# Kernel tuning notes

Hardware: AMD Instinct MI355X
Metric: run time of the kernel (lower is better)

## Reference

```python
import jax, jax.numpy as jnp
import numpy as np

DIM = 1024
HEADS = 16
B, N = 4, 2048


def setup_inputs() -> dict:
    key = jax.random.key(0)
    ks = jax.random.split(key, 6)
    scale = DIM ** -0.5
    return {
        "x": jax.random.normal(ks[0], (B, N, DIM), dtype=jnp.float32),
        "mask": jax.random.randint(ks[1], (B, N, N), 0, 2) > 0,
        "Wqkv": jax.random.normal(ks[2], (DIM, 3 * DIM), dtype=jnp.float32) * scale,
        "bqkv": jax.random.normal(ks[3], (3 * DIM,), dtype=jnp.float32) * 0.02,
        "Wproj": jax.random.normal(ks[4], (DIM, DIM), dtype=jnp.float32) * scale,
        "bproj": jax.random.normal(ks[5], (DIM,), dtype=jnp.float32) * 0.02,
    }


def reference(x, mask, Wqkv, bqkv, Wproj, bproj):
    Bs, Ns, C = x.shape
    H = HEADS
    D = C // H
    scale = D ** -0.5
    qkv = x @ Wqkv + bqkv                       # [B, N, 3C]
    qkv = qkv.reshape(Bs, Ns, 3, H, D)          # split (three h d)
    q, k, v = jnp.moveaxis(qkv, 2, 0)           # each [B, N, H, D]
    q = q.transpose(0, 2, 1, 3)                 # [B, H, N, D]
    k = k.transpose(0, 2, 1, 3)
    v = v.transpose(0, 2, 1, 3)
    attn = jnp.einsum("bhnd,bhmd->bhnm", q, k) * scale  # [B, H, N, N]
    attn = jnp.where(mask[:, None, :, :], -jnp.inf, attn)
    attn = jax.nn.softmax(attn, axis=-1)
    out = jnp.einsum("bhnm,bhmd->bhnd", attn, v)        # [B, H, N, D]
    out = out.transpose(0, 2, 1, 3).reshape(Bs, Ns, C)  # [B, N, C]
    return out @ Wproj + bproj
```

## Files before the change

### kernel.cpp

```cpp
#include <hip/hip_runtime.h>
#include <cstdint>
#include <cstddef>

constexpr int kC = 1024;
constexpr int kH = 16;
constexpr int kB = 4;
constexpr int kN = 2048;
constexpr int kD = 64;

#define KQ_SCALE 0.18033688011112042f

typedef unsigned short u16;
typedef unsigned int   u32;
typedef unsigned long long u64;
typedef __bf16 v8bf  __attribute__((ext_vector_type(8)));
typedef __bf16 v4bf  __attribute__((ext_vector_type(4)));
typedef float  v4f   __attribute__((ext_vector_type(4)));
typedef u16    u16x8 __attribute__((ext_vector_type(8)));
typedef u16    u16x4 __attribute__((ext_vector_type(4)));
typedef u32    u32x4 __attribute__((ext_vector_type(4)));

__device__ inline u16 f2bf(float f) {
    union { float f; unsigned u; } v; v.f = f;
    unsigned r = v.u + 0x7FFFu + ((v.u >> 16) & 1u);
    return (u16)(r >> 16);
}

__device__ inline float fast_exp2(float x) {
#if __has_builtin(__builtin_amdgcn_exp2f)
    return __builtin_amdgcn_exp2f(x);
#else
    return __expf(x * 0.6931471805599453f);
#endif
}

__device__ inline void gl2lds16(const u16* g, u16* l) {
    __builtin_amdgcn_global_load_lds(
        (const __attribute__((address_space(1))) void*)g,
        (__attribute__((address_space(3))) void*)l, 16, 0, 0);
}

__global__ __launch_bounds__(256) void cast_bf16_kernel(
    const float* __restrict__ in, u16* __restrict__ outp)
{
    const int i = blockIdx.x * 256 + threadIdx.x;
    const float4 f = ((const float4*)in)[i];
    u16x4 o;
    o.x = f2bf(f.x); o.y = f2bf(f.y); o.z = f2bf(f.z); o.w = f2bf(f.w);
    ((u16x4*)outp)[i] = o;
}

__global__ __launch_bounds__(256) void tpose_cast_kernel(
    const float* __restrict__ W, u16* __restrict__ Wt, int R, int Cc)
{
    __shared__ u16 tile[64][65];
    const int c0 = blockIdx.x * 64;
    const int r0 = blockIdx.y * 64;
    const int t  = threadIdx.x;
#pragma unroll
    for (int it = 0; it < 16; ++it) {
        const int r = it * 4 + (t >> 6);
        const int c = t & 63;
        tile[c][r] = f2bf(W[(size_t)(r0 + r) * Cc + c0 + c]);
    }
    __syncthreads();
#pragma unroll
    for (int it = 0; it < 16; ++it) {
        const int rr = it * 4 + (t >> 6);
        const int cc = t & 63;
        Wt[(size_t)(c0 + rr) * R + r0 + cc] = tile[rr][cc];
    }
}

__global__ __launch_bounds__(256) void maskpack_kernel(
    const int* __restrict__ mask, u32* __restrict__ bits)
{
    const int seg  = blockIdx.x * 4 + (threadIdx.x >> 6);
    const int lane = threadIdx.x & 63;
    const size_t row = (size_t)(seg >> 5);
    const int s = seg & 31;
    const int m = mask[row * kN + s * 64 + lane];
    const u64 bal = __ballot(m != 0);
    if (lane == 0) ((u64*)bits)[row * 32 + s] = bal;
}

template <int MODE>
__global__ __launch_bounds__(256) void gemm_mfma_kernel(
    const u16* __restrict__ A, const u16* __restrict__ Bt,
    const float* __restrict__ bias, float* __restrict__ Cout,
    u16* __restrict__ qOut, u16* __restrict__ kOut, u16* __restrict__ vOut,
    int M, int N, int K)
{
    __shared__ u16 As[128 * 32];
    __shared__ u16 Bs[128 * 32];
    const int t    = threadIdx.x;
    const int w    = t >> 6;
    const int lane = t & 63;
    const int quad = lane >> 4;
    const int l16  = lane & 15;
    const int m0   = blockIdx.y * 128;
    const int n0   = blockIdx.x * 128;

    const int sr = lane >> 2;
    const int sk = (lane & 3) * 8;
    const u16* Ag0 = A  + (size_t)(m0 + 32 * w      + sr) * K + sk;
    const u16* Ag1 = A  + (size_t)(m0 + 32 * w + 16 + sr) * K + sk;
    const u16* Bg0 = Bt + (size_t)(n0 + 32 * w      + sr) * K + sk;
    const u16* Bg1 = Bt + (size_t)(n0 + 32 * w + 16 + sr) * K + sk;
    u16* Al0 = &As[(32 * w)      * 32];
    u16* Al1 = &As[(32 * w + 16) * 32];
    u16* Bl0 = &Bs[(32 * w)      * 32];
    u16* Bl1 = &Bs[(32 * w + 16) * 32];

    v4f acc[4][4];
#pragma unroll
    for (int r = 0; r < 4; ++r)
#pragma unroll
        for (int c = 0; c < 4; ++c) acc[r][c] = (v4f){0.f, 0.f, 0.f, 0.f};

    const int mrow = (w >> 1) * 64;
    const int ncol = (w & 1) * 64;

    for (int k0 = 0; k0 < K; k0 += 32) {
        __syncthreads();
        gl2lds16(Ag0 + k0, Al0);
        gl2lds16(Ag1 + k0, Al1);
        gl2lds16(Bg0 + k0, Bl0);
        gl2lds16(Bg1 + k0, Bl1);
        __syncthreads();

        v8bf af[4], bfr[4];
#pragma unroll
        for (int r = 0; r < 4; ++r)
            af[r] = *(const v8bf*)(&As[(mrow + r * 16 + l16) * 32 + quad * 8]);
#pragma unroll
        for (int c = 0; c < 4; ++c)
            bfr[c] = *(const v8bf*)(&Bs[(ncol + c * 16 + l16) * 32 + quad * 8]);
#pragma unroll
        for (int r = 0; r < 4; ++r)
#pragma unroll
            for (int c = 0; c < 4; ++c)
                acc[r][c] = __builtin_amdgcn_mfma_f32_16x16x32_bf16(
                    af[r], bfr[c], acc[r][c], 0, 0, 0);
    }

#pragma unroll
    for (int r = 0; r < 4; ++r) {
#pragma unroll
        for (int c = 0; c < 4; ++c) {
            const int col = n0 + ncol + c * 16 + l16;
            const float bv = bias[col];
#pragma unroll
            for (int reg = 0; reg < 4; ++reg) {
                const int row = m0 + mrow + r * 16 + quad * 4 + reg;
                float val = acc[r][c][reg] + bv;
                if (MODE == 0) {
                    Cout[(size_t)row * N + col] = val;
                } else {
                    const int which = col >> 10;
                    const int rem   = col & 1023;
                    const int h     = rem >> 6;
                    const int d     = rem & 63;
                    const int b     = row >> 11;
                    const int n     = row & 2047;
                    if (which == 0) val *= KQ_SCALE;
                    u16* dst = (which == 0) ? qOut : (which == 1) ? kOut : vOut;
                    dst[(((size_t)(b * kH + h)) * kN + n) * kD + d] = f2bf(val);
                }
            }
        }
    }
}

__global__ __launch_bounds__(256, 2) void attn_mfma_kernel(
    const u16* __restrict__ q, const u16* __restrict__ k,
    const u16* __restrict__ v, const u32* __restrict__ mbits,
    u16* __restrict__ out)
{
    __shared__ u16 Ks[128 * 64];
    __shared__ u16 Vt[64 * 128];

    const int t    = threadIdx.x;
    const int w    = t >> 6;
    const int lane = t & 63;
    const int quad = lane >> 4;
    const int l16  = lane & 15;

    const int bh    = blockIdx.x >> 4;
    const int tile0 = (blockIdx.x & 15) * 128;
    const int b     = bh >> 4;
    const int h     = bh & 15;

    const u16* qb = q + (size_t)bh * kN * kD;
    const u16* kb = k + (size_t)bh * kN * kD;
    const u16* vb = v + (size_t)bh * kN * kD;

    const int qrow0 = tile0 + w * 32 + l16;
    const int qrow1 = qrow0 + 16;
    v8bf qf[2][2];
    qf[0][0] = *(const v8bf*)(qb + (size_t)qrow0 * kD + quad * 8);
    qf[0][1] = *(const v8bf*)(qb + (size_t)qrow0 * kD + 32 + quad * 8);
    qf[1][0] = *(const v8bf*)(qb + (size_t)qrow1 * kD + quad * 8);
    qf[1][1] = *(const v8bf*)(qb + (size_t)qrow1 * kD + 32 + quad * 8);

    const int skr  = t >> 1;
    const int skh  = t & 1;
    const int vg   = t >> 4;
    const int vdq  = t & 15;
    const int vrow0 = (vg >> 2) * 32 + (vg & 3) * 4;

    const u16* kp = kb + (size_t)skr * kD + skh * 32;
    const u16* vp = vb + (size_t)vrow0 * kD + vdq * 4;
    const uint4* mp0 = (const uint4*)(mbits + ((size_t)b * kN + qrow0) * 64);
    const uint4* mp1 = (const uint4*)(mbits + ((size_t)b * kN + qrow1) * 64);

    u16x8 kpre[4];
    u16x4 vpre[8];
    uint4 mpre0, mpre1;
    auto issue_prefetch = [&]() {
#pragma unroll
        for (int i = 0; i < 4; ++i)
            kpre[i] = *(const u16x8*)(kp + i * 8);
#pragma unroll
        for (int i = 0; i < 8; ++i)
            vpre[i] = *(const u16x4*)(vp + (i < 4 ? i * 64 : 1024 + (i - 4) * 64));
        mpre0 = *mp0; mpre1 = *mp1;
        kp += 128 * kD; vp += 128 * kD; ++mp0; ++mp1;
    };

    v8bf onesf;
#pragma unroll
    for (int j = 0; j < 8; ++j) onesf[j] = (__bf16)1.0f;

    v4f oacc[2][4];
    v4f rsacc[2];
#pragma unroll
    for (int qs = 0; qs < 2; ++qs) {
        rsacc[qs] = (v4f){0.f, 0.f, 0.f, 0.f};
#pragma unroll
        for (int i = 0; i < 4; ++i) oacc[qs][i] = (v4f){0.f, 0.f, 0.f, 0.f};
    }

    issue_prefetch();

    for (int kt = 0; kt < kN / 128; ++kt) {
        __syncthreads();

        {
            const int cb = skh * 4;
            u16* drow = &Ks[skr * 64];
#pragma unroll
            for (int i = 0; i < 4; ++i)
                *(u16x8*)(&drow[((cb + i) ^ (skr & 7)) * 8]) = kpre[i];
        }
        {
#pragma unroll
            for (int dd = 0; dd < 4; ++dd) {
                const int d = vdq * 4 + dd;
                u16x8 col;
#pragma unroll
                for (int j = 0; j < 8; ++j) col[j] = vpre[j][dd];
                *(u16x8*)(&Vt[d * 128 + ((vg ^ (d & 15)) * 8)]) = col;
            }
        }
        const uint4 mc0 = mpre0, mc1 = mpre1;
        if (kt + 1 < kN / 128) issue_prefetch();
        __syncthreads();

        const u32 mwa[2][4] = {{mc0.x, mc0.y, mc0.z, mc0.w},
                               {mc1.x, mc1.y, mc1.z, mc1.w}};
        u32 pf[2][4][4];

#pragma unroll
        for (int nb = 0; nb < 8; ++nb) {
            const int krow = nb * 16 + l16;
            const v8bf kf0 = *(const v8bf*)(&Ks[krow * 64 + ((quad       ^ (krow & 7)) * 8)]);
            const v8bf kf1 = *(const v8bf*)(&Ks[krow * 64 + (((quad + 4) ^ (krow & 7)) * 8)]);
#pragma unroll
            for (int qs = 0; qs < 2; ++qs) {
                v4f s = (v4f){0.f, 0.f, 0.f, 0.f};
                s = __builtin_amdgcn_mfma_f32_16x16x32_bf16(kf0, qf[qs][0], s, 0, 0, 0);
                s = __builtin_amdgcn_mfma_f32_16x16x32_bf16(kf1, qf[qs][1], s, 0, 0, 0);

                const u32 m4 = (mwa[qs][nb >> 1] >> ((nb & 1) * 16 + quad * 4)) & 0xFu;
                float e0 = fast_exp2(s[0]);
                float e1 = fast_exp2(s[1]);
                float e2 = fast_exp2(s[2]);
                float e3 = fast_exp2(s[3]);
                e0 = (m4 & 1u) ? 0.f : e0;
                e1 = (m4 & 2u) ? 0.f : e1;
                e2 = (m4 & 4u) ? 0.f : e2;
                e3 = (m4 & 8u) ? 0.f : e3;

                union { v4bf v; u32 u[2]; } bu;
                bu.v = (v4bf){(__bf16)e0, (__bf16)e1, (__bf16)e2, (__bf16)e3};
                pf[qs][nb >> 1][(nb & 1) * 2 + 0] = bu.u[0];
                pf[qs][nb >> 1][(nb & 1) * 2 + 1] = bu.u[1];
            }
        }

        v8bf pa[2][4];
#pragma unroll
        for (int qs = 0; qs < 2; ++qs)
#pragma unroll
            for (int ks = 0; ks < 4; ++ks) {
                u32x4 t4 = {pf[qs][ks][0], pf[qs][ks][1], pf[qs][ks][2], pf[qs][ks][3]};
                pa[qs][ks] = __builtin_bit_cast(v8bf, t4);
            }

        __builtin_amdgcn_s_setprio(1);
#pragma unroll
        for (int qs = 0; qs < 2; ++qs)
#pragma unroll
            for (int ks = 0; ks < 4; ++ks)
                rsacc[qs] = __builtin_amdgcn_mfma_f32_16x16x32_bf16(
                    pa[qs][ks], onesf, rsacc[qs], 0, 0, 0);
#pragma unroll
        for (int ks = 0; ks < 4; ++ks)
#pragma unroll
            for (int db = 0; db < 4; ++db) {
                const int d = db * 16 + l16;
                const v8bf vf = *(const v8bf*)(&Vt[d * 128 + (((ks * 4 + quad) ^ (d & 15)) * 8)]);
#pragma unroll
                for (int qs = 0; qs < 2; ++qs)
                    oacc[qs][db] = __builtin_amdgcn_mfma_f32_16x16x32_bf16(
                        pa[qs][ks], vf, oacc[qs][db], 0, 0, 0);
            }
        __builtin_amdgcn_s_setprio(0);
    }

#pragma unroll
    for (int qs = 0; qs < 2; ++qs) {
        float inv[4];
#pragma unroll
        for (int reg = 0; reg < 4; ++reg) inv[reg] = 1.f / rsacc[qs][reg];
#pragma unroll
        for (int db = 0; db < 4; ++db)
#pragma unroll
            for (int reg = 0; reg < 4; ++reg) {
                const int row = tile0 + w * 32 + qs * 16 + quad * 4 + reg;
                const int col = h * 64 + db * 16 + l16;
                out[((size_t)(b * kN + row)) * kC + col] = f2bf(oacc[qs][db][reg] * inv[reg]);
            }
    }
}

extern "C" void kernel_launch(void* const* d_in, const int* in_sizes, int n_in,
                              void* d_out, int out_size, void* d_ws, size_t ws_size,
                              hipStream_t stream)
{
    const float* x     = (const float*)d_in[0];
    const int*   mask  = (const int*)d_in[1];
    const float* Wqkv  = (const float*)d_in[2];
    const float* bqkv  = (const float*)d_in[3];
    const float* Wproj = (const float*)d_in[4];
    const float* bproj = (const float*)d_in[5];
    float* out = (float*)d_out;

    const size_t nx = (size_t)kB * kN * kC;
    const size_t qkv_elems = (size_t)kB * kH * kN * kD;
    u16* xb     = (u16*)d_ws;
    u16* qbuf   = xb + nx;
    u16* kbuf   = qbuf + qkv_elems;
    u16* vbuf   = kbuf + qkv_elems;
    u16* aob    = vbuf + qkv_elems;
    u16* Wqkvt  = aob + nx;
    u16* Wprojt = Wqkvt + (size_t)3 * kC * kC;
    u32* mbits  = (u32*)(Wprojt + (size_t)kC * kC);

    maskpack_kernel<<<dim3(kB * kN * 32 / 4), dim3(256), 0, stream>>>(mask, mbits);
    cast_bf16_kernel<<<dim3(nx / 1024), dim3(256), 0, stream>>>(x, xb);
    tpose_cast_kernel<<<dim3(3 * kC / 64, kC / 64), dim3(256), 0, stream>>>(
        Wqkv, Wqkvt, kC, 3 * kC);
    tpose_cast_kernel<<<dim3(kC / 64, kC / 64), dim3(256), 0, stream>>>(
        Wproj, Wprojt, kC, kC);

    gemm_mfma_kernel<1><<<dim3(3 * kC / 128, kB * kN / 128), dim3(256), 0, stream>>>(
        xb, Wqkvt, bqkv, nullptr, qbuf, kbuf, vbuf, kB * kN, 3 * kC, kC);

    attn_mfma_kernel<<<dim3(kB * kH * (kN / 128)), dim3(256), 0, stream>>>(
        qbuf, kbuf, vbuf, mbits, aob);

    gemm_mfma_kernel<0><<<dim3(kC / 128, kB * kN / 128), dim3(256), 0, stream>>>(
        aob, Wprojt, bproj, out, nullptr, nullptr, nullptr, kB * kN, kC, kC);
}
```

Before: 375.4 us.

## Double-buffer GEMM LDS, swizzle LDS layout, and remap blocks for XCD locality

The GEMM kernel now stages two LDS buffers so global-to-LDS loads for the next K slice overlap MFMA work on the current one, with one barrier per half-step instead of two. LDS chunks get an XOR swizzle to reduce bank conflicts, and MFMA sections run at raised wave priority. Both GEMM and attention grids are flattened and remapped so that blocks sharing operands land on the same XCD, which should improve L2 reuse. This doubles GEMM LDS use and adds a launch-bounds occupancy hint, which may raise register pressure.

```diff
diff --git a/kernel.cpp b/kernel.cpp
--- a/kernel.cpp
+++ b/kernel.cpp
@@ -85,32 +85,33 @@
 }
 
 template <int MODE>
-__global__ __launch_bounds__(256) void gemm_mfma_kernel(
+__global__ __launch_bounds__(256, 3) void gemm_mfma_kernel(
     const u16* __restrict__ A, const u16* __restrict__ Bt,
     const float* __restrict__ bias, float* __restrict__ Cout,
     u16* __restrict__ qOut, u16* __restrict__ kOut, u16* __restrict__ vOut,
     int M, int N, int K)
 {
-    __shared__ u16 As[128 * 32];
-    __shared__ u16 Bs[128 * 32];
+    __shared__ u16 As0[128 * 32], Bs0[128 * 32];
+    __shared__ u16 As1[128 * 32], Bs1[128 * 32];
     const int t    = threadIdx.x;
     const int w    = t >> 6;
     const int lane = t & 63;
     const int quad = lane >> 4;
     const int l16  = lane & 15;
-    const int m0   = blockIdx.y * 128;
-    const int n0   = blockIdx.x * 128;
-
-    const int sr = lane >> 2;
-    const int sk = (lane & 3) * 8;
-    const u16* Ag0 = A  + (size_t)(m0 + 32 * w      + sr) * K + sk;
-    const u16* Ag1 = A  + (size_t)(m0 + 32 * w + 16 + sr) * K + sk;
-    const u16* Bg0 = Bt + (size_t)(n0 + 32 * w      + sr) * K + sk;
-    const u16* Bg1 = Bt + (size_t)(n0 + 32 * w + 16 + sr) * K + sk;
-    u16* Al0 = &As[(32 * w)      * 32];
-    u16* Al1 = &As[(32 * w + 16) * 32];
-    u16* Bl0 = &Bs[(32 * w)      * 32];
-    u16* Bl1 = &Bs[(32 * w + 16) * 32];
+
+    const int nby = M >> 7;
+    const int q8  = (int)gridDim.x >> 3;
+    const int bid = (int)blockIdx.x;
+    const int swz = (bid & 7) * q8 + (bid >> 3);
+    const int m0  = (swz % nby) * 128;
+    const int n0  = (swz / nby) * 128;
+
+    const int sr  = lane >> 2;
+    const int scs = ((lane & 3) ^ ((sr >> 1) & 3)) * 8;
+    const u16* Ag0 = A  + (size_t)(m0 + 32 * w      + sr) * K + scs;
+    const u16* Ag1 = A  + (size_t)(m0 + 32 * w + 16 + sr) * K + scs;
+    const u16* Bg0 = Bt + (size_t)(n0 + 32 * w      + sr) * K + scs;
+    const u16* Bg1 = Bt + (size_t)(n0 + 32 * w + 16 + sr) * K + scs;
 
     v4f acc[4][4];
 #pragma unroll
@@ -120,28 +121,41 @@
 
     const int mrow = (w >> 1) * 64;
     const int ncol = (w & 1) * 64;
-
-    for (int k0 = 0; k0 < K; k0 += 32) {
-        __syncthreads();
-        gl2lds16(Ag0 + k0, Al0);
-        gl2lds16(Ag1 + k0, Al1);
-        gl2lds16(Bg0 + k0, Bl0);
-        gl2lds16(Bg1 + k0, Bl1);
-        __syncthreads();
-
+    const int pch  = (quad ^ ((l16 >> 1) & 3)) * 8;
+
+    auto stage = [&](u16* Asb, u16* Bsb, int k0) {
+        gl2lds16(Ag0 + k0, Asb + (32 * w) * 32);
+        gl2lds16(Ag1 + k0, Asb + (32 * w + 16) * 32);
+        gl2lds16(Bg0 + k0, Bsb + (32 * w) * 32);
+        gl2lds16(Bg1 + k0, Bsb + (32 * w + 16) * 32);
+    };
+    auto compute = [&](const u16* Asb, const u16* Bsb) {
         v8bf af[4], bfr[4];
 #pragma unroll
         for (int r = 0; r < 4; ++r)
-            af[r] = *(const v8bf*)(&As[(mrow + r * 16 + l16) * 32 + quad * 8]);
+            af[r] = *(const v8bf*)(Asb + (mrow + r * 16 + l16) * 32 + pch);
 #pragma unroll
         for (int c = 0; c < 4; ++c)
-            bfr[c] = *(const v8bf*)(&Bs[(ncol + c * 16 + l16) * 32 + quad * 8]);
+            bfr[c] = *(const v8bf*)(Bsb + (ncol + c * 16 + l16) * 32 + pch);
+        __builtin_amdgcn_s_setprio(1);
 #pragma unroll
         for (int r = 0; r < 4; ++r)
 #pragma unroll
             for (int c = 0; c < 4; ++c)
                 acc[r][c] = __builtin_amdgcn_mfma_f32_16x16x32_bf16(
                     af[r], bfr[c], acc[r][c], 0, 0, 0);
+        __builtin_amdgcn_s_setprio(0);
+    };
+
+    stage(As0, Bs0, 0);
+    __syncthreads();
+    for (int k0 = 0; k0 < K; k0 += 64) {
+        stage(As1, Bs1, k0 + 32);
+        compute(As0, Bs0);
+        __syncthreads();
+        if (k0 + 64 < K) stage(As0, Bs0, k0 + 64);
+        compute(As1, Bs1);
+        __syncthreads();
     }
 
 #pragma unroll
@@ -186,8 +200,10 @@
     const int quad = lane >> 4;
     const int l16  = lane & 15;
 
-    const int bh    = blockIdx.x >> 4;
-    const int tile0 = (blockIdx.x & 15) * 128;
+    const int bid  = (int)blockIdx.x;
+    const int swz  = (bid & 7) * 128 + (bid >> 3);
+    const int bh    = swz >> 4;
+    const int tile0 = (swz & 15) * 128;
     const int b     = bh >> 4;
     const int h     = bh & 15;
 
@@ -375,12 +391,12 @@
     tpose_cast_kernel<<<dim3(kC / 64, kC / 64), dim3(256), 0, stream>>>(
         Wproj, Wprojt, kC, kC);
 
-    gemm_mfma_kernel<1><<<dim3(3 * kC / 128, kB * kN / 128), dim3(256), 0, stream>>>(
+    gemm_mfma_kernel<1><<<dim3((3 * kC / 128) * (kB * kN / 128)), dim3(256), 0, stream>>>(
         xb, Wqkvt, bqkv, nullptr, qbuf, kbuf, vbuf, kB * kN, 3 * kC, kC);
 
     attn_mfma_kernel<<<dim3(kB * kH * (kN / 128)), dim3(256), 0, stream>>>(
         qbuf, kbuf, vbuf, mbits, aob);
 
-    gemm_mfma_kernel<0><<<dim3(kC / 128, kB * kN / 128), dim3(256), 0, stream>>>(
+    gemm_mfma_kernel<0><<<dim3((kC / 128) * (kB * kN / 128)), dim3(256), 0, stream>>>(
         aob, Wprojt, bproj, out, nullptr, nullptr, nullptr, kB * kN, kC, kC);
 }
```

New measurement: 371.8 us. Within noise of the previous version (-0.9%).
